# Kernel optimization log

Hardware: AMD Instinct MI355X
Metric: run time of the kernel (lower is better)

Reference implementation:

```python
import jax, jax.numpy as jnp
import numpy as np

B, T = 32, 1024
AC, SE, H, NH = 20, 16, 64, 4
HD = H // NH  # 16


def setup_inputs() -> dict:
    key = jax.random.key(0)
    ks = jax.random.split(key, 8)
    g = 0.1  # xavier gain used in _init_weights (rough scale)
    return {
        'acoustic': jax.random.normal(ks[0], (B, T, AC), jnp.float32),
        'semantic': jax.random.normal(ks[1], (B, T, SE), jnp.float32),
        'Wq': jax.random.normal(ks[2], (H, SE), jnp.float32) * g,
        'bq': jnp.zeros((H,), jnp.float32),
        'Wkv': jax.random.normal(ks[3], (2 * H, AC), jnp.float32) * g,
        'bkv': jnp.zeros((2 * H,), jnp.float32),
        'in_w': jax.random.normal(ks[4], (3 * H, H), jnp.float32) * g,
        'in_b': jnp.zeros((3 * H,), jnp.float32),
        'out_w': jax.random.normal(ks[5], (H, H), jnp.float32) * g,
        'out_b': jnp.zeros((H,), jnp.float32),
        'proj_w': jax.random.normal(ks[6], (AC, H), jnp.float32) * g,
        'proj_b': jnp.zeros((AC,), jnp.float32),
        'residual_logit': jnp.float32(-2.0),
        'ln_gamma': jnp.ones((AC,), jnp.float32),
        'ln_beta': jnp.zeros((AC,), jnp.float32),
    }


def _std(x, axis, keepdims=True):
    # torch.std default: unbiased (ddof=1)
    return jnp.std(x, axis=axis, ddof=1, keepdims=keepdims)


def reference(acoustic, semantic, Wq, bq, Wkv, bkv, in_w, in_b, out_w, out_b,
              proj_w, proj_b, residual_logit, ln_gamma, ln_beta):
    # projections to hidden space
    q = semantic @ Wq.T + bq                       # [B,T,H]
    kv = acoustic @ Wkv.T + bkv                    # [B,T,2H]
    k, v = kv[..., :H], kv[..., H:]
    # nn.MultiheadAttention in-projection
    qi = q @ in_w[:H].T + in_b[:H]
    ki = k @ in_w[H:2 * H].T + in_b[H:2 * H]
    vi = v @ in_w[2 * H:].T + in_b[2 * H:]
    # split heads -> [B,T,NH,HD]
    qh = qi.reshape(B, T, NH, HD)
    kh = ki.reshape(B, T, NH, HD)
    vh = vi.reshape(B, T, NH, HD)
    scores = jnp.einsum('bqhd,bkhd->bhqk', qh, kh) / jnp.sqrt(jnp.float32(HD))
    attn = jax.nn.softmax(scores, axis=-1)         # [B,NH,T,T]
    ctx = jnp.einsum('bhqk,bkhd->bqhd', attn, vh).reshape(B, T, H)
    attended = ctx @ out_w.T + out_b               # MHA out_proj
    enhanced_raw = attended @ proj_w.T + proj_b    # [B,T,AC]
    enhanced = acoustic + jax.nn.sigmoid(residual_logit) * enhanced_raw

    # statistics over batch+time (no_grad in torch -> stop_gradient)
    orig_mean = jax.lax.stop_gradient(jnp.mean(acoustic, axis=(0, 1), keepdims=True))
    orig_std = jax.lax.stop_gradient(_std(acoustic, (0, 1)) + 1e-8)
    a_n = (acoustic - orig_mean) / orig_std
    e_n = (enhanced - orig_mean) / orig_std
    std_ratio = _std(e_n, (0, 1)) / (_std(a_n, (0, 1)) + 1e-8)
    std_corr = jnp.where(std_ratio < 0.4, 0.4 / std_ratio, jnp.ones_like(std_ratio))
    enhanced_final = (e_n * std_corr) * orig_std + orig_mean

    # LayerNorm over last dim (biased variance, eps=1e-5)
    mu = jnp.mean(enhanced_final, axis=-1, keepdims=True)
    var = jnp.mean(jnp.square(enhanced_final - mu), axis=-1, keepdims=True)
    return (enhanced_final - mu) * jax.lax.rsqrt(var + 1e-5) * ln_gamma + ln_beta
```

## Files before the change

kernel.cpp:

```cpp
#include <hip/hip_runtime.h>
#include <hip/hip_bf16.h>
#include <math.h>

#define B 32
#define T 1024
#define AC 20
#define SE 16
#define H 64
#define NH 4
#define HD 16
#define NROW (B*T)
#define BH (B*NH)
#define KS 2
#define KSLICE (T/KS)
#define NCH (KSLICE/32)

typedef unsigned short u16;
typedef short short8 __attribute__((ext_vector_type(8)));
typedef float floatx4 __attribute__((ext_vector_type(4)));

#define F_QB   (BH*T*16/2)
#define OFF_QB   0
#define OFF_KB   (OFF_QB + F_QB)
#define OFF_VT   (OFF_KB + F_QB)
#define OFF_PART (OFF_VT + F_QB)
#define OFF_PARTL (OFF_PART + KS*BH*T*16)
#define OFF_ET   (OFF_PARTL + KS*BH*T)
#define OFF_AT   (OFF_ET + AC*NROW)
#define OFF_WF   (OFF_AT + AC*NROW)
#define OFF_PST  (OFF_WF + 5120)
#define OFF_ACC  (OFF_PST + 20*16*4)

#define WF_WQ 0
#define WF_BQ 1024
#define WF_WK 1088
#define WF_BK 2368
#define WF_WV 2432
#define WF_BV 3712
#define WF_WO 3776
#define WF_BO 5056
#define WF_TOTAL 5076

__device__ __forceinline__ u16 bf16b(float a) {
    __hip_bfloat16 t = __float2bfloat16(a);
    u16 u; __builtin_memcpy(&u, &t, 2); return u;
}
__device__ __forceinline__ unsigned packbf(float a, float b) {
    return (unsigned)bf16b(a) | ((unsigned)bf16b(b) << 16);
}

__global__ __launch_bounds__(256) void k_fuse(
    const float* __restrict__ Wq, const float* __restrict__ bq,
    const float* __restrict__ Wkv, const float* __restrict__ bkv,
    const float* __restrict__ in_w, const float* __restrict__ in_b,
    const float* __restrict__ out_w, const float* __restrict__ out_b,
    const float* __restrict__ proj_w, const float* __restrict__ proj_b,
    float* __restrict__ wf) {
    int idx = blockIdx.x * 256 + threadIdx.x;
    if (idx >= WF_TOTAL) return;
    if (idx < WF_BQ) {
        int i = idx >> 4, j = idx & 15;
        float s = 0.f;
        for (int m = 0; m < H; ++m) s += in_w[i*H + m] * Wq[m*SE + j];
        wf[idx] = 0.25f * s;
    } else if (idx < WF_WK) {
        int i = idx - WF_BQ;
        float s = in_b[i];
        for (int m = 0; m < H; ++m) s += in_w[i*H + m] * bq[m];
        wf[idx] = 0.25f * s;
    } else if (idx < WF_BK) {
        int r = idx - WF_WK; int i = r / AC, j = r % AC;
        float s = 0.f;
        for (int m = 0; m < H; ++m) s += in_w[(H+i)*H + m] * Wkv[m*AC + j];
        wf[idx] = s;
    } else if (idx < WF_WV) {
        int i = idx - WF_BK;
        float s = in_b[H + i];
        for (int m = 0; m < H; ++m) s += in_w[(H+i)*H + m] * bkv[m];
        wf[idx] = s;
    } else if (idx < WF_BV) {
        int r = idx - WF_WV; int i = r / AC, j = r % AC;
        float s = 0.f;
        for (int m = 0; m < H; ++m) s += in_w[(2*H+i)*H + m] * Wkv[(H+m)*AC + j];
        wf[idx] = s;
    } else if (idx < WF_WO) {
        int i = idx - WF_BV;
        float s = in_b[2*H + i];
        for (int m = 0; m < H; ++m) s += in_w[(2*H+i)*H + m] * bkv[H + m];
        wf[idx] = s;
    } else if (idx < WF_BO) {
        int r = idx - WF_WO; int c = r >> 6, d = r & 63;
        float s = 0.f;
        for (int m = 0; m < H; ++m) s += proj_w[c*H + m] * out_w[m*H + d];
        wf[idx] = s;
    } else {
        int c = idx - WF_BO;
        float s = proj_b[c];
        for (int m = 0; m < H; ++m) s += proj_w[c*H + m] * out_b[m];
        wf[idx] = s;
    }
}

__global__ __launch_bounds__(192) void k_qkv(
    const float* __restrict__ sem, const float* __restrict__ acst,
    const float* __restrict__ wf,
    u16* __restrict__ Qb, u16* __restrict__ Kb, u16* __restrict__ Vtb) {
    const int tid = threadIdx.x;
    const int sec = tid >> 4, r = tid & 15;
    const int row = blockIdx.x * 16 + r;
    const int b = row >> 10, t = row & 1023;
    const int type = sec >> 2, h = sec & 3;
    float o[16];
    if (type == 0) {
        float s[SE];
        const float4* sp = (const float4*)(sem + (size_t)row * SE);
        #pragma unroll
        for (int i = 0; i < 4; ++i) {
            float4 v = sp[i];
            s[4*i] = v.x; s[4*i+1] = v.y; s[4*i+2] = v.z; s[4*i+3] = v.w;
        }
        const float* wq = wf + WF_WQ + h*16*SE;
        const float* bq = wf + WF_BQ + h*16;
        #pragma unroll
        for (int ii = 0; ii < 16; ++ii) {
            float acc = bq[ii];
            #pragma unroll
            for (int j = 0; j < 4; ++j) {
                float4 w4 = *(const float4*)(wq + ii*SE + 4*j);
                acc += s[4*j]*w4.x + s[4*j+1]*w4.y + s[4*j+2]*w4.z + s[4*j+3]*w4.w;
            }
            o[ii] = acc;
        }
        unsigned* dst = (unsigned*)(Qb + (((size_t)(b*NH + h))*T + t)*16);
        #pragma unroll
        for (int i = 0; i < 8; ++i) dst[i] = packbf(o[2*i], o[2*i+1]);
    } else {
        float a[AC];
        const float4* ap = (const float4*)(acst + (size_t)row * AC);
        #pragma unroll
        for (int i = 0; i < 5; ++i) {
            float4 v = ap[i];
            a[4*i] = v.x; a[4*i+1] = v.y; a[4*i+2] = v.z; a[4*i+3] = v.w;
        }
        const float* wb = wf + (type == 1 ? WF_WK : WF_WV) + h*16*AC;
        const float* bb = wf + (type == 1 ? WF_BK : WF_BV) + h*16;
        #pragma unroll
        for (int ii = 0; ii < 16; ++ii) {
            float acc = bb[ii];
            #pragma unroll
            for (int j = 0; j < 5; ++j) {
                float4 w4 = *(const float4*)(wb + ii*AC + 4*j);
                acc += a[4*j]*w4.x + a[4*j+1]*w4.y + a[4*j+2]*w4.z + a[4*j+3]*w4.w;
            }
            o[ii] = acc;
        }
        if (type == 1) {
            unsigned* dst = (unsigned*)(Kb + (((size_t)(b*NH + h))*T + t)*16);
            #pragma unroll
            for (int i = 0; i < 8; ++i) dst[i] = packbf(o[2*i], o[2*i+1]);
        } else {
            int w32 = t & 31;
            int slot = (w32 < 16) ? (w32*2) : ((w32-16)*2 + 1);
            int tp = (t & ~31) | slot;
            #pragma unroll
            for (int d = 0; d < HD; ++d)
                Vtb[((size_t)(b*NH + h)*16 + d)*T + tp] = bf16b(o[d]);
        }
    }
}

#define KPAD 24
#define VROW 528
__global__ __launch_bounds__(256) void k_attn(
    const u16* __restrict__ Qb, const u16* __restrict__ Kb, const u16* __restrict__ Vtb,
    float* __restrict__ part, float* __restrict__ partL) {
    __shared__ __align__(16) u16 Ks[KSLICE*KPAD];
    __shared__ __align__(16) u16 Vs[16*VROW];
    __shared__ __align__(16) u16 Ps[4*16*40];
    const int tid = threadIdx.x;
    const int blk = blockIdx.x;
    const int ks = blk & 1;
    const int qb = (blk >> 1) & 15;
    const int bh = blk >> 5;
    const int kbase = ks * KSLICE;
    {
        const uint4* src = (const uint4*)(Kb + ((size_t)bh*T + kbase)*16);
        for (int r = tid; r < KSLICE; r += 256) {
            uint4 a0 = src[2*r], a1 = src[2*r + 1];
            *(uint4*)&Ks[r*KPAD]     = a0;
            *(uint4*)&Ks[r*KPAD + 8] = a1;
        }
        for (int i = tid; i < 16*(KSLICE/8); i += 256) {
            int d = i >> 6, c = i & 63;
            uint4 v = *(const uint4*)(Vtb + ((size_t)(bh*16 + d))*T + kbase + c*8);
            *(uint4*)&Vs[d*VROW + c*8] = v;
        }
    }
    __syncthreads();
    const int wv = tid >> 6, lane = tid & 63;
    const int col = lane & 15, quad = lane >> 4;
    const int q0 = qb*64 + wv*16;
    short8 qf = {0,0,0,0,0,0,0,0};
    if (quad < 2)
        qf = *(const short8*)(Qb + ((size_t)bh*T + q0 + col)*16 + quad*8);
    const floatx4 z4 = {0.f,0.f,0.f,0.f};
    floatx4 acc = z4;
    float ls[4] = {0.f,0.f,0.f,0.f};
    u16* Pw = &Ps[wv*640];
    for (int ch = 0; ch < NCH; ++ch) {
        short8 kf0 = {0,0,0,0,0,0,0,0}, kf1 = {0,0,0,0,0,0,0,0};
        if (quad < 2) {
            kf0 = *(const short8*)&Ks[(ch*32 + col)*KPAD + quad*8];
            kf1 = *(const short8*)&Ks[(ch*32 + 16 + col)*KPAD + quad*8];
        }
        floatx4 s0 = __builtin_amdgcn_mfma_f32_16x16x32_bf16(qf, kf0, z4, 0, 0, 0);
        floatx4 s1 = __builtin_amdgcn_mfma_f32_16x16x32_bf16(qf, kf1, z4, 0, 0, 0);
        float p0[4], p1[4];
        #pragma unroll
        for (int r = 0; r < 4; ++r) {
            p0[r] = __expf(s0[r]); p1[r] = __expf(s1[r]);
            ls[r] += p0[r] + p1[r];
        }
        #pragma unroll
        for (int r = 0; r < 4; ++r)
            *(unsigned*)&Pw[(quad*4 + r)*40 + col*2] = packbf(p0[r], p1[r]);
        short8 pf = *(const short8*)&Pw[col*40 + quad*8];
        short8 vf = *(const short8*)&Vs[col*VROW + ch*32 + quad*8];
        acc = __builtin_amdgcn_mfma_f32_16x16x32_bf16(pf, vf, acc, 0, 0, 0);
    }
    float* dst = part + (((size_t)ks*BH + bh)*T + q0)*16;
    #pragma unroll
    for (int r = 0; r < 4; ++r) dst[(quad*4 + r)*16 + col] = acc[r];
    #pragma unroll
    for (int m = 1; m < 16; m <<= 1) {
        #pragma unroll
        for (int r = 0; r < 4; ++r) ls[r] += __shfl_xor(ls[r], m);
    }
    if (col == 0) {
        float* ld = partL + ((size_t)ks*BH + bh)*T + q0 + quad*4;
        #pragma unroll
        for (int r = 0; r < 4; ++r) ld[r] = ls[r];
    }
}

#define CSTR 65
__global__ __launch_bounds__(256) void k_proj(
    const float* __restrict__ part, const float* __restrict__ partL,
    const float* __restrict__ acst, const float* __restrict__ wf,
    const float* __restrict__ rlogit,
    float* __restrict__ enhT, float* __restrict__ aT) {
    __shared__ float ctxs[64*CSTR];
    __shared__ __align__(16) float wsm[AC*H + AC];
    const int tid = threadIdx.x;
    for (int i = tid; i < AC*H + AC; i += 256) wsm[i] = wf[WF_WO + i];
    {
        const int r = tid & 63, h = tid >> 6;
        const int row = blockIdx.x*64 + r;
        const int b = row >> 10, t = row & 1023;
        const int bh = b*NH + h;
        float l = partL[(size_t)bh*T + t] + partL[(size_t)(BH + bh)*T + t];
        float inv = 1.f / l;
        const float4* pa = (const float4*)(part + ((size_t)bh*T + t)*16);
        const float4* pb = (const float4*)(part + ((size_t)(BH + bh)*T + t)*16);
        float* cd = &ctxs[r*CSTR + h*16];
        #pragma unroll
        for (int i = 0; i < 4; ++i) {
            float4 x = pa[i], y = pb[i];
            cd[4*i+0] = (x.x + y.x)*inv;
            cd[4*i+1] = (x.y + y.y)*inv;
            cd[4*i+2] = (x.z + y.z)*inv;
            cd[4*i+3] = (x.w + y.w)*inv;
        }
    }
    __syncthreads();
    const int r = tid & 63, cg = tid >> 6;
    const int row = blockIdx.x*64 + r;
    float c64[H];
    #pragma unroll
    for (int k = 0; k < H; ++k) c64[k] = ctxs[r*CSTR + k];
    float sg = 1.f / (1.f + __expf(-rlogit[0]));
    #pragma unroll
    for (int j = 0; j < 5; ++j) {
        int ch = cg*5 + j;
        float s = wsm[AC*H + ch];
        const float4* w4 = (const float4*)(wsm + ch*H);
        #pragma unroll
        for (int k = 0; k < 16; ++k) {
            float4 w = w4[k];
            s += c64[4*k]*w.x + c64[4*k+1]*w.y + c64[4*k+2]*w.z + c64[4*k+3]*w.w;
        }
        float a = acst[(size_t)row*AC + ch];
        float e = a + sg * s;
        enhT[(size_t)ch * NROW + row] = e;
        aT[(size_t)ch * NROW + row]  = a;
    }
}

__global__ __launch_bounds__(256) void k_stats1(
    const float* __restrict__ aT, const float* __restrict__ enhT,
    float* __restrict__ pst) {
    int c = blockIdx.x >> 4, sl = blockIdx.x & 15;
    int base = sl * (NROW/16);
    const float* ac = aT  + (size_t)c*NROW + base;
    const float* ec = enhT + (size_t)c*NROW + base;
    float sa = 0.f, qa = 0.f, se = 0.f, qe = 0.f;
    for (int r = threadIdx.x; r < NROW/16; r += 256) {
        float a = ac[r]; sa += a; qa += a*a;
        float e = ec[r]; se += e; qe += e*e;
    }
    #pragma unroll
    for (int off = 32; off > 0; off >>= 1) {
        sa += __shfl_down(sa, off);
        qa += __shfl_down(qa, off);
        se += __shfl_down(se, off);
        qe += __shfl_down(qe, off);
    }
    __shared__ float rs[4][4];
    int w = threadIdx.x >> 6;
    if ((threadIdx.x & 63) == 0) { rs[w][0] = sa; rs[w][1] = qa; rs[w][2] = se; rs[w][3] = qe; }
    __syncthreads();
    if (threadIdx.x == 0) {
        float A = 0.f, QA = 0.f, E = 0.f, QE = 0.f;
        for (int i = 0; i < 4; ++i) { A += rs[i][0]; QA += rs[i][1]; E += rs[i][2]; QE += rs[i][3]; }
        float* d = pst + (size_t)(c*16 + sl)*4;
        d[0] = A; d[1] = QA; d[2] = E; d[3] = QE;
    }
}

__global__ __launch_bounds__(128) void k_stats2(
    const float* __restrict__ pst, float* __restrict__ accum) {
    int i = threadIdx.x;
    if (i < 80) {
        int c = i >> 2, j = i & 3;
        float s = 0.f;
        for (int sl = 0; sl < 16; ++sl) s += pst[(size_t)(c*16 + sl)*4 + j];
        accum[i] = s;
    }
}

__global__ __launch_bounds__(128) void k_final(
    const float* __restrict__ enhT, const float* __restrict__ accum,
    const float* __restrict__ gamma, const float* __restrict__ beta,
    float* __restrict__ out) {
    int row = blockIdx.x * 128 + threadIdx.x;
    const float Nf = (float)NROW;
    float ef[AC];
    #pragma unroll
    for (int c = 0; c < AC; ++c) {
        float sa = accum[c*4+0], qa = accum[c*4+1];
        float se = accum[c*4+2], qe = accum[c*4+3];
        float mu  = sa / Nf;
        float va  = (qa - sa*sa/Nf) / (Nf - 1.f);
        float sda = sqrtf(fmaxf(va, 0.f));
        float osd = sda + 1e-8f;
        float ve  = (qe - se*se/Nf) / (Nf - 1.f);
        float sde = sqrtf(fmaxf(ve, 0.f));
        float ratio = (sde / osd) / (sda / osd + 1e-8f);
        float corr  = (ratio < 0.4f) ? (0.4f / ratio) : 1.f;
        float e = enhT[(size_t)c * NROW + row];
        ef[c] = (e - mu) * corr + mu;
    }
    float m = 0.f;
    #pragma unroll
    for (int c = 0; c < AC; ++c) m += ef[c];
    m *= (1.f / AC);
    float v = 0.f;
    #pragma unroll
    for (int c = 0; c < AC; ++c) { float d = ef[c] - m; v += d*d; }
    v *= (1.f / AC);
    float inv = rsqrtf(v + 1e-5f);
    float o[AC];
    #pragma unroll
    for (int c = 0; c < AC; ++c) o[c] = (ef[c] - m) * inv * gamma[c] + beta[c];
    float4* op = (float4*)(out + (size_t)row * AC);
    #pragma unroll
    for (int i = 0; i < 5; ++i)
        op[i] = make_float4(o[4*i], o[4*i+1], o[4*i+2], o[4*i+3]);
}

extern "C" void kernel_launch(void* const* d_in, const int* in_sizes, int n_in,
                              void* d_out, int out_size, void* d_ws, size_t ws_size,
                              hipStream_t stream) {
    (void)in_sizes; (void)n_in; (void)out_size; (void)ws_size;
    const float* acoustic = (const float*)d_in[0];
    const float* semantic = (const float*)d_in[1];
    const float* Wq     = (const float*)d_in[2];
    const float* bq     = (const float*)d_in[3];
    const float* Wkv    = (const float*)d_in[4];
    const float* bkv    = (const float*)d_in[5];
    const float* in_w   = (const float*)d_in[6];
    const float* in_b   = (const float*)d_in[7];
    const float* out_w  = (const float*)d_in[8];
    const float* out_b  = (const float*)d_in[9];
    const float* proj_w = (const float*)d_in[10];
    const float* proj_b = (const float*)d_in[11];
    const float* rlogit = (const float*)d_in[12];
    const float* gamma  = (const float*)d_in[13];
    const float* beta   = (const float*)d_in[14];
    float* ws = (float*)d_ws;
    u16* Qb  = (u16*)(ws + OFF_QB);
    u16* Kb  = (u16*)(ws + OFF_KB);
    u16* Vtb = (u16*)(ws + OFF_VT);
    float* part  = ws + OFF_PART;
    float* partL = ws + OFF_PARTL;
    float* enhT  = ws + OFF_ET;
    float* aT    = ws + OFF_AT;
    float* wf    = ws + OFF_WF;
    float* pst   = ws + OFF_PST;
    float* accum = ws + OFF_ACC;
    float* out = (float*)d_out;

    k_fuse<<<(WF_TOTAL + 255)/256, 256, 0, stream>>>(Wq, bq, Wkv, bkv, in_w, in_b,
                                                     out_w, out_b, proj_w, proj_b, wf);
    k_qkv<<<NROW/16, 192, 0, stream>>>(semantic, acoustic, wf, Qb, Kb, Vtb);
    k_attn<<<BH*16*KS, 256, 0, stream>>>(Qb, Kb, Vtb, part, partL);
    k_proj<<<NROW/64, 256, 0, stream>>>(part, partL, acoustic, wf, rlogit, enhT, aT);
    k_stats1<<<AC*16, 256, 0, stream>>>(aT, enhT, pst);
    k_stats2<<<1, 128, 0, stream>>>(pst, accum);
    k_final<<<NROW/128, 128, 0, stream>>>(enhT, accum, gamma, beta, out);
}
```

Measured before the change: 168.7 us.

## Rewrite attention with 32x32 MFMA, register P via permlane swap, no split-K

The attention kernel switches from 16x16x32 MFMAs staged through LDS to 32x32x16 MFMAs whose operands are read straight from global memory, with the next chunk prefetched into registers. The softmax probabilities are rearranged in registers with v_permlane32_swap instead of a shared-memory round trip. V is stored in a new blocked layout to match. The key-dimension split and its partial-sum merge are removed, so the kernel writes normalized context transposed for k_proj to read directly. The separate stats2 launch is also folded into k_final. The costs are LDS traffic and extra kernel launches; the risks are lower parallelism (1024 blocks instead of 4096) and more global-memory pressure from K/V loads that are no longer shared through LDS.

New measurement: 158.5 us. 1.06x faster.

```diff
diff --git a/kernel.cpp b/kernel.cpp
--- a/kernel.cpp
+++ b/kernel.cpp
@@ -12,12 +12,13 @@
 #define NROW (B*T)
 #define BH (B*NH)
 #define KS 2
-#define KSLICE (T/KS)
-#define NCH (KSLICE/32)
+#define NCHUNK (T/32)
 
 typedef unsigned short u16;
 typedef short short8 __attribute__((ext_vector_type(8)));
 typedef float floatx4 __attribute__((ext_vector_type(4)));
+typedef float f32x16 __attribute__((ext_vector_type(16)));
+typedef unsigned int uintx4 __attribute__((ext_vector_type(4)));
 
 #define F_QB   (BH*T*16/2)
 #define OFF_QB   0
@@ -159,122 +160,101 @@
             #pragma unroll
             for (int i = 0; i < 8; ++i) dst[i] = packbf(o[2*i], o[2*i+1]);
         } else {
-            int w32 = t & 31;
-            int slot = (w32 < 16) ? (w32*2) : ((w32-16)*2 + 1);
-            int tp = (t & ~31) | slot;
+            u16* dst = Vtb + ((size_t)(b*NH + h)*64 + (t >> 4))*256 + (t & 15);
             #pragma unroll
-            for (int d = 0; d < HD; ++d)
-                Vtb[((size_t)(b*NH + h)*16 + d)*T + tp] = bf16b(o[d]);
-        }
-    }
-}
-
-#define KPAD 24
-#define VROW 528
-__global__ __launch_bounds__(256) void k_attn(
+            for (int d = 0; d < HD; ++d) dst[d*16] = bf16b(o[d]);
+        }
+    }
+}
+
+__global__ __launch_bounds__(256, 4) void k_attn(
     const u16* __restrict__ Qb, const u16* __restrict__ Kb, const u16* __restrict__ Vtb,
-    float* __restrict__ part, float* __restrict__ partL) {
-    __shared__ __align__(16) u16 Ks[KSLICE*KPAD];
-    __shared__ __align__(16) u16 Vs[16*VROW];
-    __shared__ __align__(16) u16 Ps[4*16*40];
-    const int tid = threadIdx.x;
-    const int blk = blockIdx.x;
-    const int ks = blk & 1;
-    const int qb = (blk >> 1) & 15;
-    const int bh = blk >> 5;
-    const int kbase = ks * KSLICE;
-    {
-        const uint4* src = (const uint4*)(Kb + ((size_t)bh*T + kbase)*16);
-        for (int r = tid; r < KSLICE; r += 256) {
-            uint4 a0 = src[2*r], a1 = src[2*r + 1];
-            *(uint4*)&Ks[r*KPAD]     = a0;
-            *(uint4*)&Ks[r*KPAD + 8] = a1;
-        }
-        for (int i = tid; i < 16*(KSLICE/8); i += 256) {
-            int d = i >> 6, c = i & 63;
-            uint4 v = *(const uint4*)(Vtb + ((size_t)(bh*16 + d))*T + kbase + c*8);
-            *(uint4*)&Vs[d*VROW + c*8] = v;
-        }
-    }
-    __syncthreads();
-    const int wv = tid >> 6, lane = tid & 63;
-    const int col = lane & 15, quad = lane >> 4;
-    const int q0 = qb*64 + wv*16;
-    short8 qf = {0,0,0,0,0,0,0,0};
-    if (quad < 2)
-        qf = *(const short8*)(Qb + ((size_t)bh*T + q0 + col)*16 + quad*8);
-    const floatx4 z4 = {0.f,0.f,0.f,0.f};
-    floatx4 acc = z4;
-    float ls[4] = {0.f,0.f,0.f,0.f};
-    u16* Pw = &Ps[wv*640];
-    for (int ch = 0; ch < NCH; ++ch) {
-        short8 kf0 = {0,0,0,0,0,0,0,0}, kf1 = {0,0,0,0,0,0,0,0};
-        if (quad < 2) {
-            kf0 = *(const short8*)&Ks[(ch*32 + col)*KPAD + quad*8];
-            kf1 = *(const short8*)&Ks[(ch*32 + 16 + col)*KPAD + quad*8];
-        }
-        floatx4 s0 = __builtin_amdgcn_mfma_f32_16x16x32_bf16(qf, kf0, z4, 0, 0, 0);
-        floatx4 s1 = __builtin_amdgcn_mfma_f32_16x16x32_bf16(qf, kf1, z4, 0, 0, 0);
-        float p0[4], p1[4];
-        #pragma unroll
-        for (int r = 0; r < 4; ++r) {
-            p0[r] = __expf(s0[r]); p1[r] = __expf(s1[r]);
-            ls[r] += p0[r] + p1[r];
-        }
-        #pragma unroll
-        for (int r = 0; r < 4; ++r)
-            *(unsigned*)&Pw[(quad*4 + r)*40 + col*2] = packbf(p0[r], p1[r]);
-        short8 pf = *(const short8*)&Pw[col*40 + quad*8];
-        short8 vf = *(const short8*)&Vs[col*VROW + ch*32 + quad*8];
-        acc = __builtin_amdgcn_mfma_f32_16x16x32_bf16(pf, vf, acc, 0, 0, 0);
-    }
-    float* dst = part + (((size_t)ks*BH + bh)*T + q0)*16;
-    #pragma unroll
-    for (int r = 0; r < 4; ++r) dst[(quad*4 + r)*16 + col] = acc[r];
-    #pragma unroll
-    for (int m = 1; m < 16; m <<= 1) {
-        #pragma unroll
-        for (int r = 0; r < 4; ++r) ls[r] += __shfl_xor(ls[r], m);
-    }
-    if (col == 0) {
-        float* ld = partL + ((size_t)ks*BH + bh)*T + q0 + quad*4;
-        #pragma unroll
-        for (int r = 0; r < 4; ++r) ld[r] = ls[r];
+    float* __restrict__ ctxT) {
+    const int tid  = threadIdx.x;
+    const int lane = tid & 63;
+    const int wv   = tid >> 6;
+    const int blk  = blockIdx.x;
+    const int bh   = blk & 127;
+    const int qblk = blk >> 7;
+    const int b = bh >> 2, h = bh & 3;
+    const int l31 = lane & 31, hi2 = lane >> 5, l15 = lane & 15;
+    const int q0 = qblk*128 + wv*32;
+
+    const short8 qf = *(const short8*)(Qb + ((size_t)bh*T + q0 + l31)*16 + 8*hi2);
+    const u16* kp = Kb + ((size_t)bh*T + l31)*16 + 8*hi2;
+    const u16* vp = Vtb + (size_t)bh*16384 + l15*16 + 8*hi2;
+
+    f32x16 acc = {0.f,0.f,0.f,0.f,0.f,0.f,0.f,0.f,0.f,0.f,0.f,0.f,0.f,0.f,0.f,0.f};
+    const f32x16 z16 = {0.f,0.f,0.f,0.f,0.f,0.f,0.f,0.f,0.f,0.f,0.f,0.f,0.f,0.f,0.f,0.f};
+    float ls = 0.f;
+
+    short8 kf = *(const short8*)kp;
+    short8 va = *(const short8*)vp;
+    short8 vb = *(const short8*)(vp + 256);
+    #pragma unroll 4
+    for (int ch = 0; ch < NCHUNK; ++ch) {
+        const int nx = (ch < NCHUNK-1) ? ch + 1 : ch;
+        short8 kf_n = *(const short8*)(kp + (size_t)nx*512);
+        short8 va_n = *(const short8*)(vp + (size_t)nx*512);
+        short8 vb_n = *(const short8*)(vp + (size_t)nx*512 + 256);
+
+        f32x16 sc = __builtin_amdgcn_mfma_f32_32x32x16_bf16(kf, qf, z16, 0, 0, 0);
+        float p[16];
+        #pragma unroll
+        for (int r = 0; r < 16; ++r) p[r] = __expf(sc[r]);
+        #pragma unroll
+        for (int r = 0; r < 16; ++r) ls += p[r];
+
+        unsigned u0 = packbf(p[0],  p[1]);
+        unsigned u1 = packbf(p[2],  p[3]);
+        unsigned u2 = packbf(p[4],  p[5]);
+        unsigned u3 = packbf(p[6],  p[7]);
+        unsigned u4 = packbf(p[8],  p[9]);
+        unsigned u5 = packbf(p[10], p[11]);
+        unsigned u6 = packbf(p[12], p[13]);
+        unsigned u7 = packbf(p[14], p[15]);
+        asm("v_permlane32_swap_b32 %0, %1" : "+v"(u2), "+v"(u0));
+        asm("v_permlane32_swap_b32 %0, %1" : "+v"(u3), "+v"(u1));
+        asm("v_permlane32_swap_b32 %0, %1" : "+v"(u6), "+v"(u4));
+        asm("v_permlane32_swap_b32 %0, %1" : "+v"(u7), "+v"(u5));
+        uintx4 t1 = {u0, u1, u2, u3};
+        uintx4 t2 = {u4, u5, u6, u7};
+        short8 pf1 = __builtin_bit_cast(short8, t1);
+        short8 pf2 = __builtin_bit_cast(short8, t2);
+
+        acc = __builtin_amdgcn_mfma_f32_32x32x16_bf16(va, pf1, acc, 0, 0, 0);
+        acc = __builtin_amdgcn_mfma_f32_32x32x16_bf16(vb, pf2, acc, 0, 0, 0);
+
+        kf = kf_n; va = va_n; vb = vb_n;
+    }
+
+    ls += __shfl_xor(ls, 32);
+    const float inv = 1.f / ls;
+    const int row = b*T + q0 + l31;
+    #pragma unroll
+    for (int r = 0; r < 8; ++r) {
+        const int d = (r & 3) + 8*(r >> 2) + 4*hi2;
+        ctxT[(size_t)(h*16 + d)*NROW + row] = acc[r] * inv;
     }
 }
 
 #define CSTR 65
 __global__ __launch_bounds__(256) void k_proj(
-    const float* __restrict__ part, const float* __restrict__ partL,
-    const float* __restrict__ acst, const float* __restrict__ wf,
-    const float* __restrict__ rlogit,
+    const float* __restrict__ ctxT, const float* __restrict__ acst,
+    const float* __restrict__ wf, const float* __restrict__ rlogit,
     float* __restrict__ enhT, float* __restrict__ aT) {
     __shared__ float ctxs[64*CSTR];
     __shared__ __align__(16) float wsm[AC*H + AC];
     const int tid = threadIdx.x;
     for (int i = tid; i < AC*H + AC; i += 256) wsm[i] = wf[WF_WO + i];
-    {
-        const int r = tid & 63, h = tid >> 6;
-        const int row = blockIdx.x*64 + r;
-        const int b = row >> 10, t = row & 1023;
-        const int bh = b*NH + h;
-        float l = partL[(size_t)bh*T + t] + partL[(size_t)(BH + bh)*T + t];
-        float inv = 1.f / l;
-        const float4* pa = (const float4*)(part + ((size_t)bh*T + t)*16);
-        const float4* pb = (const float4*)(part + ((size_t)(BH + bh)*T + t)*16);
-        float* cd = &ctxs[r*CSTR + h*16];
-        #pragma unroll
-        for (int i = 0; i < 4; ++i) {
-            float4 x = pa[i], y = pb[i];
-            cd[4*i+0] = (x.x + y.x)*inv;
-            cd[4*i+1] = (x.y + y.y)*inv;
-            cd[4*i+2] = (x.z + y.z)*inv;
-            cd[4*i+3] = (x.w + y.w)*inv;
-        }
+    const int row0 = blockIdx.x * 64;
+    for (int i = tid; i < 64*64; i += 256) {
+        int ch = i >> 6, rr = i & 63;
+        ctxs[rr*CSTR + ch] = ctxT[(size_t)ch*NROW + row0 + rr];
     }
     __syncthreads();
     const int r = tid & 63, cg = tid >> 6;
-    const int row = blockIdx.x*64 + r;
+    const int row = row0 + r;
     float c64[H];
     #pragma unroll
     for (int k = 0; k < H; ++k) c64[k] = ctxs[r*CSTR + k];
@@ -327,28 +307,27 @@
     }
 }
 
-__global__ __launch_bounds__(128) void k_stats2(
-    const float* __restrict__ pst, float* __restrict__ accum) {
-    int i = threadIdx.x;
-    if (i < 80) {
-        int c = i >> 2, j = i & 3;
-        float s = 0.f;
-        for (int sl = 0; sl < 16; ++sl) s += pst[(size_t)(c*16 + sl)*4 + j];
-        accum[i] = s;
-    }
-}
-
 __global__ __launch_bounds__(128) void k_final(
-    const float* __restrict__ enhT, const float* __restrict__ accum,
+    const float* __restrict__ enhT, const float* __restrict__ pst,
     const float* __restrict__ gamma, const float* __restrict__ beta,
     float* __restrict__ out) {
-    int row = blockIdx.x * 128 + threadIdx.x;
+    __shared__ float acs[80];
+    const int tx = threadIdx.x;
+    if (tx < 80) {
+        int c = tx >> 2, j = tx & 3;
+        float s = 0.f;
+        #pragma unroll
+        for (int sl = 0; sl < 16; ++sl) s += pst[(size_t)(c*16 + sl)*4 + j];
+        acs[tx] = s;
+    }
+    __syncthreads();
+    int row = blockIdx.x * 128 + tx;
     const float Nf = (float)NROW;
     float ef[AC];
     #pragma unroll
     for (int c = 0; c < AC; ++c) {
-        float sa = accum[c*4+0], qa = accum[c*4+1];
-        float se = accum[c*4+2], qe = accum[c*4+3];
+        float sa = acs[c*4+0], qa = acs[c*4+1];
+        float se = acs[c*4+2], qe = acs[c*4+3];
         float mu  = sa / Nf;
         float va  = (qa - sa*sa/Nf) / (Nf - 1.f);
         float sda = sqrtf(fmaxf(va, 0.f));
@@ -401,21 +380,18 @@
     u16* Qb  = (u16*)(ws + OFF_QB);
     u16* Kb  = (u16*)(ws + OFF_KB);
     u16* Vtb = (u16*)(ws + OFF_VT);
-    float* part  = ws + OFF_PART;
-    float* partL = ws + OFF_PARTL;
+    float* ctxT  = ws + OFF_PART;
     float* enhT  = ws + OFF_ET;
     float* aT    = ws + OFF_AT;
     float* wf    = ws + OFF_WF;
     float* pst   = ws + OFF_PST;
-    float* accum = ws + OFF_ACC;
     float* out = (float*)d_out;
 
     k_fuse<<<(WF_TOTAL + 255)/256, 256, 0, stream>>>(Wq, bq, Wkv, bkv, in_w, in_b,
                                                      out_w, out_b, proj_w, proj_b, wf);
     k_qkv<<<NROW/16, 192, 0, stream>>>(semantic, acoustic, wf, Qb, Kb, Vtb);
-    k_attn<<<BH*16*KS, 256, 0, stream>>>(Qb, Kb, Vtb, part, partL);
-    k_proj<<<NROW/64, 256, 0, stream>>>(part, partL, acoustic, wf, rlogit, enhT, aT);
+    k_attn<<<8*BH, 256, 0, stream>>>(Qb, Kb, Vtb, ctxT);
+    k_proj<<<NROW/64, 256, 0, stream>>>(ctxT, acoustic, wf, rlogit, enhT, aT);
     k_stats1<<<AC*16, 256, 0, stream>>>(aT, enhT, pst);
-    k_stats2<<<1, 128, 0, stream>>>(pst, accum);
-    k_final<<<NROW/128, 128, 0, stream>>>(enhT, accum, gamma, beta, out);
-}
+    k_final<<<NROW/128, 128, 0, stream>>>(enhT, pst, gamma, beta, out);
+}
```
